# Kernel optimization log

Measured on AMD Instinct MI355X. Metric: run time of the kernel, lower is better.

Reference implementation:

```python
import jax, jax.numpy as jnp
import numpy as np

N, E, D, C, H1 = 50000, 800000, 128, 8, 2


def setup_inputs() -> dict:
    key = jax.random.key(0)
    ks = jax.random.split(key, 14)
    s = lambda k, sh: (jax.random.normal(k, sh, jnp.float32) * 0.05)
    return {
        "x": jax.random.normal(ks[0], (N, D), jnp.float32),
        "edge_index": jax.random.randint(ks[1], (2, E), 0, N, dtype=jnp.int32),
        # conv1: GATConv(D, D, heads=2, concat=True)
        "W1": s(ks[2], (D, H1 * D)),
        "att1_src": s(ks[3], (H1, D)),
        "att1_dst": s(ks[4], (H1, D)),
        "b1": s(ks[5], (H1 * D,)),
        # conv2: GATConv(2D, D, heads=1, concat=False)
        "W2": s(ks[6], (H1 * D, D)),
        "att2_src": s(ks[7], (1, D)),
        "att2_dst": s(ks[8], (1, D)),
        "b2": s(ks[9], (D,)),
        # MLP head
        "Wm1": s(ks[10], (D, D)),
        "bm1": s(ks[11], (D,)),
        "Wm2": s(ks[12], (D, C)),
        "bm2": s(ks[13], (C,)),
    }


def gat_conv(x, src, dst, W, a_src, a_dst, b, heads, out_ch, concat):
    """PyG GATConv (eval mode): self-loops added by caller, softmax over
    edges grouped by destination node, negative_slope=0.2."""
    n = x.shape[0]
    h = (x @ W).reshape(n, heads, out_ch)              # [N,H,F]
    alpha_src = jnp.einsum('nhf,hf->nh', h, a_src)     # [N,H]
    alpha_dst = jnp.einsum('nhf,hf->nh', h, a_dst)     # [N,H]
    e = jax.nn.leaky_relu(alpha_src[src] + alpha_dst[dst], 0.2)  # [E,H]
    e_max = jax.ops.segment_max(e, dst, num_segments=n)
    ex = jnp.exp(e - e_max[dst])
    denom = jax.ops.segment_sum(ex, dst, num_segments=n)
    alpha = ex / jnp.maximum(denom[dst], 1e-16)        # [E,H]
    out = jax.ops.segment_sum(h[src] * alpha[:, :, None], dst, num_segments=n)
    out = out.reshape(n, heads * out_ch) if concat else out.mean(axis=1)
    return out + b


def reference(x, edge_index, W1, att1_src, att1_dst, b1,
              W2, att2_src, att2_dst, b2, Wm1, bm1, Wm2, bm2):
    n = x.shape[0]
    loop = jnp.arange(n, dtype=edge_index.dtype)
    src = jnp.concatenate([edge_index[0], loop])  # add_self_loops=True
    dst = jnp.concatenate([edge_index[1], loop])
    h = jax.nn.elu(gat_conv(x, src, dst, W1, att1_src, att1_dst, b1, H1, D, True))
    h = jax.nn.elu(gat_conv(h, src, dst, W2, att2_src, att2_dst, b2, 1, D, False))
    h = jax.nn.relu(h @ Wm1 + bm1)
    return jax.nn.relu(h @ Wm2 + bm2)
```

## Files before the change

### kernel.cpp

```cpp
#include <hip/hip_runtime.h>
#include <hip/hip_bf16.h>


__device__ __forceinline__ float lrelu(float x){ return x > 0.f ? x : 0.2f*x; }
__device__ __forceinline__ float elu_f(float x){ return x > 0.f ? x : __expf(x) - 1.f; }
__device__ __forceinline__ unsigned short f2bf(float f){
  __hip_bfloat16 h = __float2bfloat16(f);
  return *reinterpret_cast<unsigned short*>(&h);
}
__device__ __forceinline__ float bflo(unsigned int u){ return __uint_as_float(u << 16); }
__device__ __forceinline__ float bfhi(unsigned int u){ return __uint_as_float(u & 0xffff0000u); }
__device__ __forceinline__ unsigned int packbf(float a, float b){
  return (unsigned int)f2bf(a) | ((unsigned int)f2bf(b) << 16);
}

typedef __attribute__((ext_vector_type(8))) short bf16x8;
typedef __attribute__((ext_vector_type(4))) float f32x4;

__global__ void prep_kernel(const float* __restrict__ W1, unsigned short* __restrict__ BT1a,
                            unsigned short* __restrict__ BT1b,
                            const float* __restrict__ W2, unsigned short* __restrict__ BT2,
                            const float* __restrict__ Wm1, unsigned short* __restrict__ BT3,
                            const float* __restrict__ a1s, const float* __restrict__ a1d,
                            float* __restrict__ va, int* __restrict__ bcount,
                            int* __restrict__ gcur, int NB){
  int idx = blockIdx.x*256 + threadIdx.x;
  const int S1 = 128*256, S2 = 128*256, S3 = 128*128;
  if (idx < S1){
    int k = idx >> 8, c = idx & 255;
    unsigned short v = f2bf(W1[idx]);
    if (c < 128) BT1a[c*128 + k] = v;
    else         BT1b[(c-128)*128 + k] = v;
  } else if (idx < S1 + S2){
    int j = idx - S1;
    int k = j >> 7, n = j & 127;
    BT2[n*256 + k] = f2bf(W2[j]);
  } else if (idx < S1 + S2 + S3){
    int j = idx - S1 - S2;
    int k = j >> 7, n = j & 127;
    BT3[n*128 + k] = f2bf(Wm1[j]);
  } else if (idx < S1 + S2 + S3 + 512){
    int j = idx - S1 - S2 - S3;
    int v = j >> 7, k = j & 127;
    const float* avec = (v < 2) ? a1s : a1d;
    int head = v & 1;
    const float4* wrow = (const float4*)(W1 + (size_t)k*256 + head*128);
    const float4* arow = (const float4*)(avec + head*128);
    float s = 0.f;
    #pragma unroll 8
    for (int f = 0; f < 32; ++f){
      float4 w = wrow[f], a = arow[f];
      s += w.x*a.x + w.y*a.y + w.z*a.z + w.w*a.w;
    }
    va[j] = s;
  } else if (idx < S1 + S2 + S3 + 512 + 2048){
    int z = idx - (S1 + S2 + S3 + 512);
    if (z < 1024){ if (z < NB) bcount[z] = 0; }
    else { z -= 1024; if (z < NB) gcur[z] = 0; }
  }
}

__global__ __launch_bounds__(256) void f2bf_hist_kernel(
    const float* __restrict__ x, unsigned short* __restrict__ xb, int N,
    const float* __restrict__ va, float* __restrict__ as1, float* __restrict__ ad1,
    const int* __restrict__ dst, int E, int* __restrict__ bcount, int NB, int nbConv)
{
  __shared__ int h[1024];
  if ((int)blockIdx.x < nbConv){
    int i = blockIdx.x*256 + threadIdx.x;
    int total = N*32;
    float4 v = make_float4(0.f,0.f,0.f,0.f);
    if (i < total){
      v = ((const float4*)x)[i];
      ushort4 u; u.x=f2bf(v.x); u.y=f2bf(v.y); u.z=f2bf(v.z); u.w=f2bf(v.w);
      ((ushort4*)xb)[i] = u;
    }
    int c = (i & 31) << 2;
    float4 vs0 = *(const float4*)(va + c);
    float4 vs1 = *(const float4*)(va + 128 + c);
    float4 vd0 = *(const float4*)(va + 256 + c);
    float4 vd1 = *(const float4*)(va + 384 + c);
    float s0 = v.x*vs0.x + v.y*vs0.y + v.z*vs0.z + v.w*vs0.w;
    float s1 = v.x*vs1.x + v.y*vs1.y + v.z*vs1.z + v.w*vs1.w;
    float d0 = v.x*vd0.x + v.y*vd0.y + v.z*vd0.z + v.w*vd0.w;
    float d1 = v.x*vd1.x + v.y*vd1.y + v.z*vd1.z + v.w*vd1.w;
    #pragma unroll
    for (int m = 1; m <= 16; m <<= 1){
      s0 += __shfl_xor(s0, m); s1 += __shfl_xor(s1, m);
      d0 += __shfl_xor(d0, m); d1 += __shfl_xor(d1, m);
    }
    if ((i & 31) == 0 && i < total){
      int n = i >> 5;
      *(float2*)(as1 + 2*n) = make_float2(s0, s1);
      *(float2*)(ad1 + 2*n) = make_float2(d0, d1);
    }
  } else {
    for (int i = threadIdx.x; i < NB; i += 256) h[i] = 0;
    __syncthreads();
    int b0 = blockIdx.x - nbConv;
    for (int e = b0*256 + threadIdx.x; e < E; e += 64*256)
      atomicAdd(&h[dst[e] >> 6], 1);
    __syncthreads();
    for (int i = threadIdx.x; i < NB; i += 256)
      if (h[i]) atomicAdd(&bcount[i], h[i]);
  }
}

__global__ __launch_bounds__(256) void bscatter_kernel(
    const int* __restrict__ src, const int* __restrict__ dst, int E,
    const int* __restrict__ bcount, int* __restrict__ boff,
    int* __restrict__ gcur, unsigned int* __restrict__ pairs, int NB)
{
  __shared__ int h[1024];
  __shared__ int runbase[1024];
  __shared__ int sc[1024];
  const int t = threadIdx.x;
  const int e0 = blockIdx.x * 4096;

  for (int i = t; i < 1024; i += 256) sc[i] = (i < NB) ? bcount[i] : 0;
  for (int i = t; i < NB; i += 256) h[i] = 0;
  __syncthreads();
  for (int d = 1; d < 1024; d <<= 1){
    int v0 = (t       >= d) ? sc[t       - d] : 0;
    int v1 = (t + 256 >= d) ? sc[t + 256 - d] : 0;
    int v2 = (t + 512 >= d) ? sc[t + 512 - d] : 0;
    int v3 = (t + 768 >= d) ? sc[t + 768 - d] : 0;
    __syncthreads();
    sc[t] += v0; sc[t+256] += v1; sc[t+512] += v2; sc[t+768] += v3;
    __syncthreads();
  }
  if (blockIdx.x == 0){
    for (int i = t; i <= NB; i += 256) boff[i] = i ? sc[i-1] : 0;
  }

  int myb[16]; unsigned int myw[16];
  #pragma unroll
  for (int q = 0; q < 16; ++q){
    int e = e0 + q*256 + t;
    int b = -1; unsigned int w = 0;
    if (e < E){
      int d = dst[e];
      b = d >> 6;
      w = ((unsigned int)(d & 63) << 26) | (unsigned int)src[e];
      atomicAdd(&h[b], 1);
    }
    myb[q] = b; myw[q] = w;
  }
  __syncthreads();
  for (int i = t; i < NB; i += 256)
    runbase[i] = h[i] ? atomicAdd(&gcur[i], h[i]) : 0;
  __syncthreads();
  for (int i = t; i < NB; i += 256) h[i] = 0;
  __syncthreads();
  #pragma unroll
  for (int q = 0; q < 16; ++q){
    if (myb[q] >= 0){
      int off = atomicAdd(&h[myb[q]], 1);
      int base = myb[q] ? sc[myb[q]-1] : 0;
      pairs[(size_t)base + runbase[myb[q]] + off] = myw[q];
    }
  }
}

__global__ __launch_bounds__(256) void bbuild_kernel(
    const unsigned int* __restrict__ pairs, const int* __restrict__ boff,
    int* __restrict__ rowptr, int* __restrict__ csr, int N)
{
  __shared__ int deg[64], offs[64], cur[64];
  const int b = blockIdx.x;
  const int t = threadIdx.x;
  const int n0 = b << 6;
  const int nNodes = min(64, N - n0);
  const int p0 = boff[b], p1 = boff[b+1];
  const int base = p0 + n0;
  if (t < 64) deg[t] = (t < nNodes) ? 1 : 0;
  __syncthreads();
  for (int i = p0 + t; i < p1; i += 256)
    atomicAdd(&deg[pairs[i] >> 26], 1);
  __syncthreads();
  if (t < 64){
    int x = deg[t];
    #pragma unroll
    for (int d = 1; d < 64; d <<= 1){
      int y = __shfl_up(x, d);
      if (t >= d) x += y;
    }
    offs[t] = x - deg[t];
    cur[t] = 1;
    if (t < nNodes){
      rowptr[n0 + t + 1] = base + x;
      csr[base + x - deg[t]] = n0 + t;
    }
    if (b == 0 && t == 0) rowptr[0] = 0;
  }
  __syncthreads();
  for (int i = p0 + t; i < p1; i += 256){
    unsigned int w = pairs[i];
    int dl = w >> 26;
    int s  = (int)(w & 0x03ffffffu);
    int off = atomicAdd(&cur[dl], 1);
    csr[base + offs[dl] + off] = s;
  }
}

__device__ __forceinline__ void gemm_core(
    const unsigned short* __restrict__ A, int lda,
    const unsigned short* __restrict__ BT, int M, int K, int r0,
    unsigned short* a_s, unsigned short* b_s, f32x4 (&acc)[4][4])
{
  const int tid  = threadIdx.x;
  const int lane = tid & 63, wv = tid >> 6;
  const int mh = (wv & 1)*64, nh = (wv >> 1)*64;
  const int l15 = lane & 15, quad = lane >> 4;
  const int srow = tid >> 3, skc = tid & 7;

  #pragma unroll
  for (int i = 0; i < 4; ++i)
    #pragma unroll
    for (int j = 0; j < 4; ++j)
      #pragma unroll
      for (int r = 0; r < 4; ++r) acc[i][j][r] = 0.f;

  for (int k0 = 0; k0 < K; k0 += 64){
    #pragma unroll
    for (int it = 0; it < 4; ++it){
      int row = it*32 + srow;
      int grow = r0 + row;
      uint4 v = make_uint4(0u,0u,0u,0u);
      if (grow < M) v = *(const uint4*)(A + (size_t)grow*lda + k0 + skc*8);
      *(uint4*)(&a_s[row*72 + skc*8]) = v;
    }
    #pragma unroll
    for (int it = 0; it < 4; ++it){
      int row = it*32 + srow;
      uint4 v = *(const uint4*)(BT + (size_t)row*K + k0 + skc*8);
      *(uint4*)(&b_s[row*72 + skc*8]) = v;
    }
    __syncthreads();
    #pragma unroll
    for (int ks = 0; ks < 64; ks += 32){
      bf16x8 af[4], bfr[4];
      #pragma unroll
      for (int i = 0; i < 4; ++i)
        af[i] = *(const bf16x8*)(&a_s[(mh + i*16 + l15)*72 + ks + quad*8]);
      #pragma unroll
      for (int j = 0; j < 4; ++j)
        bfr[j] = *(const bf16x8*)(&b_s[(nh + j*16 + l15)*72 + ks + quad*8]);
      #pragma unroll
      for (int i = 0; i < 4; ++i)
        #pragma unroll
        for (int j = 0; j < 4; ++j)
          acc[i][j] = __builtin_amdgcn_mfma_f32_16x16x32_bf16(bfr[j], af[i], acc[i][j], 0, 0, 0);
    }
    __syncthreads();
  }
}

__global__ __launch_bounds__(256) void gemm_conv1_kernel(
    const unsigned short* __restrict__ xa, const unsigned short* __restrict__ BT1a,
    const unsigned short* __restrict__ BT1b, unsigned short* __restrict__ out1b,
    int M, const float* __restrict__ b1)
{
  __shared__ unsigned short a_s[128*72];
  __shared__ unsigned short b_s[128*72];
  const int hx = blockIdx.x;
  const unsigned short* A  = xa + hx*128;
  const unsigned short* BT = hx ? BT1b : BT1a;
  unsigned short* C = out1b + hx*128;
  const float* bias = b1 + hx*128;
  const int r0 = blockIdx.y*128;
  f32x4 acc[4][4];
  gemm_core(A, 256, BT, M, 128, r0, a_s, b_s, acc);

  const int lane = threadIdx.x & 63, wv = threadIdx.x >> 6;
  const int mh = (wv & 1)*64, nh = (wv >> 1)*64;
  const int l15 = lane & 15, quad = lane >> 4;
  #pragma unroll
  for (int i = 0; i < 4; ++i){
    int m = r0 + mh + i*16 + l15;
    if (m < M){
      #pragma unroll
      for (int j = 0; j < 4; ++j){
        int n = nh + j*16 + quad*4;
        float4 bb = *(const float4*)(bias + n);
        ushort4 u;
        u.x = f2bf(elu_f(acc[i][j][0] + bb.x));
        u.y = f2bf(elu_f(acc[i][j][1] + bb.y));
        u.z = f2bf(elu_f(acc[i][j][2] + bb.z));
        u.w = f2bf(elu_f(acc[i][j][3] + bb.w));
        *(ushort4*)(C + (size_t)m*256 + n) = u;
      }
    }
  }
}

__global__ __launch_bounds__(256) void gemm_conv2_kernel(
    const unsigned short* __restrict__ out1b, const unsigned short* __restrict__ BT2,
    unsigned short* __restrict__ h2b, int M,
    const float* __restrict__ a2s, const float* __restrict__ a2d,
    float* __restrict__ as2, float* __restrict__ ad2)
{
  __shared__ unsigned short a_s[128*72];
  __shared__ unsigned short b_s[128*72];
  __shared__ float part_s[128][2];
  __shared__ float part_d[128][2];
  const int r0 = blockIdx.y*128;
  f32x4 acc[4][4];
  gemm_core(out1b, 256, BT2, M, 256, r0, a_s, b_s, acc);

  const int tid = threadIdx.x;
  const int lane = tid & 63, wv = tid >> 6;
  const int mh = (wv & 1)*64, nh = (wv >> 1)*64;
  const int l15 = lane & 15, quad = lane >> 4;
  #pragma unroll
  for (int i = 0; i < 4; ++i){
    int m = r0 + mh + i*16 + l15;
    float ps = 0.f, pd = 0.f;
    #pragma unroll
    for (int j = 0; j < 4; ++j){
      int n = nh + j*16 + quad*4;
      float4 wsv = *(const float4*)(a2s + n);
      float4 wdv = *(const float4*)(a2d + n);
      float v0 = acc[i][j][0], v1 = acc[i][j][1], v2 = acc[i][j][2], v3 = acc[i][j][3];
      ps += v0*wsv.x + v1*wsv.y + v2*wsv.z + v3*wsv.w;
      pd += v0*wdv.x + v1*wdv.y + v2*wdv.z + v3*wdv.w;
      if (m < M){
        ushort4 u;
        u.x = f2bf(v0); u.y = f2bf(v1); u.z = f2bf(v2); u.w = f2bf(v3);
        *(ushort4*)(h2b + (size_t)m*128 + n) = u;
      }
    }
    ps += __shfl_xor(ps, 16); ps += __shfl_xor(ps, 32);
    pd += __shfl_xor(pd, 16); pd += __shfl_xor(pd, 32);
    if (quad == 0){
      part_s[mh + i*16 + l15][wv >> 1] = ps;
      part_d[mh + i*16 + l15][wv >> 1] = pd;
    }
  }
  __syncthreads();
  if (tid < 128){
    int gm = r0 + tid;
    if (gm < M){
      as2[gm] = part_s[tid][0] + part_s[tid][1];
      ad2[gm] = part_d[tid][0] + part_d[tid][1];
    }
  }
}

__global__ __launch_bounds__(256) void gemm_mlp_kernel(
    const unsigned short* __restrict__ gb, const unsigned short* __restrict__ BT3,
    int M, const float* __restrict__ bm1, const float* __restrict__ Wm2,
    const float* __restrict__ bm2, float* __restrict__ out)
{
  __shared__ unsigned short a_s[128*72];
  __shared__ unsigned short b_s[128*72];
  __shared__ float wm2_s[128*8];
  __shared__ float part[128][2][8];
  const int tid = threadIdx.x;
  {
    int i4 = tid*4;
    *(float4*)(&wm2_s[i4]) = *(const float4*)(Wm2 + i4);
  }
  const int r0 = blockIdx.y*128;
  f32x4 acc[4][4];
  gemm_core(gb, 128, BT3, M, 128, r0, a_s, b_s, acc);

  const int lane = tid & 63, wv = tid >> 6;
  const int mh = (wv & 1)*64, nh = (wv >> 1)*64;
  const int l15 = lane & 15, quad = lane >> 4;
  #pragma unroll
  for (int i = 0; i < 4; ++i){
    float po[8];
    #pragma unroll
    for (int o = 0; o < 8; ++o) po[o] = 0.f;
    #pragma unroll
    for (int j = 0; j < 4; ++j){
      int n = nh + j*16 + quad*4;
      float4 bb = *(const float4*)(bm1 + n);
      #pragma unroll
      for (int r = 0; r < 4; ++r){
        float hcol = fmaxf(acc[i][j][r] + ((const float*)&bb)[r], 0.f);
        const float* wr = &wm2_s[(n + r)*8];
        #pragma unroll
        for (int o = 0; o < 8; ++o) po[o] += hcol*wr[o];
      }
    }
    #pragma unroll
    for (int o = 0; o < 8; ++o){
      po[o] += __shfl_xor(po[o], 16);
      po[o] += __shfl_xor(po[o], 32);
    }
    if (quad == 0){
      #pragma unroll
      for (int o = 0; o < 8; ++o) part[mh + i*16 + l15][wv >> 1][o] = po[o];
    }
  }
  __syncthreads();
  if (tid < 128){
    int gm = r0 + tid;
    if (gm < M){
      float4 o0, o1;
      o0.x = fmaxf(part[tid][0][0] + part[tid][1][0] + bm2[0], 0.f);
      o0.y = fmaxf(part[tid][0][1] + part[tid][1][1] + bm2[1], 0.f);
      o0.z = fmaxf(part[tid][0][2] + part[tid][1][2] + bm2[2], 0.f);
      o0.w = fmaxf(part[tid][0][3] + part[tid][1][3] + bm2[3], 0.f);
      o1.x = fmaxf(part[tid][0][4] + part[tid][1][4] + bm2[4], 0.f);
      o1.y = fmaxf(part[tid][0][5] + part[tid][1][5] + bm2[5], 0.f);
      o1.z = fmaxf(part[tid][0][6] + part[tid][1][6] + bm2[6], 0.f);
      o1.w = fmaxf(part[tid][0][7] + part[tid][1][7] + bm2[7], 0.f);
      *(float4*)(out + (size_t)gm*8)     = o0;
      *(float4*)(out + (size_t)gm*8 + 4) = o1;
    }
  }
}

#define AGG1_FMA(u, a0v, a1v) do{ \
    float f0 = bflo(u.x), f1 = bfhi(u.x), f2v = bflo(u.y), f3 = bfhi(u.y); \
    float f4 = bflo(u.z), f5 = bfhi(u.z), f6 = bflo(u.w), f7 = bfhi(u.w); \
    acc0[0] += a0v*f0; acc0[1] += a0v*f1; acc0[2] += a0v*f2v; acc0[3] += a0v*f3; \
    acc0[4] += a0v*f4; acc0[5] += a0v*f5; acc0[6] += a0v*f6;  acc0[7] += a0v*f7; \
    acc1[0] += a1v*f0; acc1[1] += a1v*f1; acc1[2] += a1v*f2v; acc1[3] += a1v*f3; \
    acc1[4] += a1v*f4; acc1[5] += a1v*f5; acc1[6] += a1v*f6;  acc1[7] += a1v*f7; \
  }while(0)

#define AGG2_FMA(u, av) do{ \
    acc[0] += av*bflo(u.x); acc[1] += av*bfhi(u.x); \
    acc[2] += av*bflo(u.y); acc[3] += av*bfhi(u.y); \
    acc[4] += av*bflo(u.z); acc[5] += av*bfhi(u.z); \
    acc[6] += av*bflo(u.w); acc[7] += av*bfhi(u.w); \
  }while(0)

__global__ __launch_bounds__(256) void agg1x_kernel(
    const unsigned short* __restrict__ xb, const float* __restrict__ as_,
    const float* __restrict__ ad_, const int* __restrict__ rowptr, const int* __restrict__ csr,
    unsigned short* __restrict__ xa, int N)
{
  const int wv = threadIdx.x >> 6, lane = threadIdx.x & 63;
  const int ql = lane & 15;
  const int n = blockIdx.x*16 + wv*4 + (lane >> 4);
  const bool valid = n < N;
  int start = 0, end = 0;
  float2 adv = make_float2(0.f, 0.f);
  if (valid){ start = rowptr[n]; end = rowptr[n+1]; adv = *(const float2*)(ad_ + 2*n); }

  int jl = start + ql;
  bool have = valid && (jl < end);
  int s_l = 0;
  float p0 = 0.f, p1 = 0.f;
  if (have){
    s_l = csr[jl];
    float2 av = *(const float2*)(as_ + 2*s_l);
    p0 = __expf(lrelu(av.x + adv.x));
    p1 = __expf(lrelu(av.y + adv.y));
  }
  float l0 = p0, l1 = p1;
  for (int j = jl + 16; j < end; j += 16){
    int s = csr[j];
    float2 av = *(const float2*)(as_ + 2*s);
    l0 += __expf(lrelu(av.x + adv.x));
    l1 += __expf(lrelu(av.y + adv.y));
  }
  #pragma unroll
  for (int msk = 1; msk <= 8; msk <<= 1){
    l0 += __shfl_xor(l0, msk);
    l1 += __shfl_xor(l1, msk);
  }
  float inv0 = 1.f / fmaxf(l0, 1e-16f);
  float inv1 = 1.f / fmaxf(l1, 1e-16f);
  float a0_l = p0 * inv0;
  float a1_l = p1 * inv1;

  float acc0[8], acc1[8];
  #pragma unroll
  for (int i = 0; i < 8; ++i){ acc0[i] = 0.f; acc1[i] = 0.f; }
  const int c = ql << 3;
  const unsigned short* hp = xb + c;

  #pragma unroll
  for (int t = 0; t < 16; t += 2){
    int   sA  = __shfl(s_l, t, 16),   sB  = __shfl(s_l, t+1, 16);
    float a0A = __shfl(a0_l, t, 16),  a0B = __shfl(a0_l, t+1, 16);
    float a1A = __shfl(a1_l, t, 16),  a1B = __shfl(a1_l, t+1, 16);
    uint4 uA = *(const uint4*)(hp + (sA << 7));
    uint4 uB = *(const uint4*)(hp + (sB << 7));
    AGG1_FMA(uA, a0A, a1A);
    AGG1_FMA(uB, a0B, a1B);
  }
  for (int jb = start + 16; jb < end; jb += 16){
    int jl2 = jb + ql;
    int s2 = 0; float a0_2 = 0.f, a1_2 = 0.f;
    if (jl2 < end){
      s2 = csr[jl2];
      float2 av = *(const float2*)(as_ + 2*s2);
      a0_2 = __expf(lrelu(av.x + adv.x)) * inv0;
      a1_2 = __expf(lrelu(av.y + adv.y)) * inv1;
    }
    int cnt2 = min(16, end - jb);
    for (int t2 = 0; t2 < cnt2; t2 += 2){
      int   sA  = __shfl(s2, t2, 16),   sB  = __shfl(s2, t2+1, 16);
      float a0A = __shfl(a0_2, t2, 16), a0B = __shfl(a0_2, t2+1, 16);
      float a1A = __shfl(a1_2, t2, 16), a1B = __shfl(a1_2, t2+1, 16);
      uint4 uA = *(const uint4*)(hp + (sA << 7));
      uint4 uB = *(const uint4*)(hp + (sB << 7));
      AGG1_FMA(uA, a0A, a1A);
      AGG1_FMA(uB, a0B, a1B);
    }
  }

  if (valid){
    uint4 u0, u1;
    u0.x = packbf(acc0[0], acc0[1]); u0.y = packbf(acc0[2], acc0[3]);
    u0.z = packbf(acc0[4], acc0[5]); u0.w = packbf(acc0[6], acc0[7]);
    u1.x = packbf(acc1[0], acc1[1]); u1.y = packbf(acc1[2], acc1[3]);
    u1.z = packbf(acc1[4], acc1[5]); u1.w = packbf(acc1[6], acc1[7]);
    *(uint4*)(xa + (size_t)n*256 + c)       = u0;
    *(uint4*)(xa + (size_t)n*256 + 128 + c) = u1;
  }
}

__global__ __launch_bounds__(256) void agg2_kernel(
    const unsigned short* __restrict__ h2b, const float* __restrict__ as_,
    const float* __restrict__ ad_, const int* __restrict__ rowptr, const int* __restrict__ csr,
    const float* __restrict__ b2, unsigned short* __restrict__ outb, int N)
{
  const int wv = threadIdx.x >> 6, lane = threadIdx.x & 63;
  const int ql = lane & 15;
  const int n = blockIdx.x*16 + wv*4 + (lane >> 4);
  const bool valid = n < N;
  int start = 0, end = 0;
  float adn = 0.f;
  if (valid){ start = rowptr[n]; end = rowptr[n+1]; adn = ad_[n]; }

  int jl = start + ql;
  bool have = valid && (jl < end);
  int s_l = 0;
  float p_l = 0.f;
  if (have){
    s_l = csr[jl];
    p_l = __expf(lrelu(as_[s_l] + adn));
  }
  float l = p_l;
  for (int j = jl + 16; j < end; j += 16)
    l += __expf(lrelu(as_[csr[j]] + adn));
  #pragma unroll
  for (int msk = 1; msk <= 8; msk <<= 1) l += __shfl_xor(l, msk);
  float inv = 1.f / fmaxf(l, 1e-16f);
  float a_l = p_l * inv;

  float acc[8];
  #pragma unroll
  for (int i = 0; i < 8; ++i) acc[i] = 0.f;
  const int c = ql << 3;
  const unsigned short* hp = h2b + c;

  #pragma unroll
  for (int t = 0; t < 16; t += 2){
    int   sA = __shfl(s_l, t, 16),  sB = __shfl(s_l, t+1, 16);
    float aA = __shfl(a_l, t, 16),  aB = __shfl(a_l, t+1, 16);
    uint4 uA = *(const uint4*)(hp + (sA << 7));
    uint4 uB = *(const uint4*)(hp + (sB << 7));
    AGG2_FMA(uA, aA);
    AGG2_FMA(uB, aB);
  }
  for (int jb = start + 16; jb < end; jb += 16){
    int jl2 = jb + ql;
    int s2 = 0; float a2 = 0.f;
    if (jl2 < end){
      s2 = csr[jl2];
      a2 = __expf(lrelu(as_[s2] + adn)) * inv;
    }
    int cnt2 = min(16, end - jb);
    for (int t2 = 0; t2 < cnt2; t2 += 2){
      int   sA = __shfl(s2, t2, 16),  sB = __shfl(s2, t2+1, 16);
      float aA = __shfl(a2, t2, 16),  aB = __shfl(a2, t2+1, 16);
      uint4 uA = *(const uint4*)(hp + (sA << 7));
      uint4 uB = *(const uint4*)(hp + (sB << 7));
      AGG2_FMA(uA, aA);
      AGG2_FMA(uB, aB);
    }
  }

  if (valid){
    float4 bb0 = *(const float4*)(b2 + c);
    float4 bb1 = *(const float4*)(b2 + c + 4);
    float o[8];
    o[0]=elu_f(acc[0]+bb0.x); o[1]=elu_f(acc[1]+bb0.y);
    o[2]=elu_f(acc[2]+bb0.z); o[3]=elu_f(acc[3]+bb0.w);
    o[4]=elu_f(acc[4]+bb1.x); o[5]=elu_f(acc[5]+bb1.y);
    o[6]=elu_f(acc[6]+bb1.z); o[7]=elu_f(acc[7]+bb1.w);
    uint4 up;
    up.x = packbf(o[0], o[1]); up.y = packbf(o[2], o[3]);
    up.z = packbf(o[4], o[5]); up.w = packbf(o[6], o[7]);
    *(uint4*)(outb + (size_t)n*128 + c) = up;
  }
}

extern "C" void kernel_launch(void* const* d_in, const int* in_sizes, int n_in,
                              void* d_out, int out_size, void* d_ws, size_t ws_size,
                              hipStream_t stream)
{
  (void)n_in; (void)out_size; (void)ws_size;
  const float* x   = (const float*)d_in[0];
  const int*   ei  = (const int*)d_in[1];
  const float* W1  = (const float*)d_in[2];
  const float* a1s = (const float*)d_in[3];
  const float* a1d = (const float*)d_in[4];
  const float* b1  = (const float*)d_in[5];
  const float* W2  = (const float*)d_in[6];
  const float* a2s = (const float*)d_in[7];
  const float* a2d = (const float*)d_in[8];
  const float* b2  = (const float*)d_in[9];
  const float* Wm1 = (const float*)d_in[10];
  const float* bm1 = (const float*)d_in[11];
  const float* Wm2 = (const float*)d_in[12];
  const float* bm2 = (const float*)d_in[13];
  float* out = (float*)d_out;

  const int N = in_sizes[0] / 128;
  const int E = in_sizes[1] / 2;
  const int NB = (N + 63) >> 6;
  const int* srcp = ei;
  const int* dstp = ei + E;

  char* ws = (char*)d_ws;
  unsigned short* xb    = (unsigned short*)ws;
  unsigned short* xa    = (unsigned short*)(ws + (size_t)N*256);
  unsigned short* out1b = (unsigned short*)(ws + (size_t)N*768);
  unsigned short* h2b   = (unsigned short*)(ws + (size_t)N*1280);
  char* tail = ws + (size_t)N*1536;
  unsigned short* BT1a = (unsigned short*)tail;
  unsigned short* BT1b = BT1a + 128*128;
  unsigned short* BT2  = BT1b + 128*128;
  unsigned short* BT3  = BT2 + 128*256;
  float* va   = (float*)(BT3 + 128*128);
  float* as1  = va + 512;
  float* ad1  = as1 + (size_t)2*N;
  float* as2  = ad1 + (size_t)2*N;
  float* ad2  = as2 + N;
  int* bcount = (int*)(ad2 + N);
  int* boff   = bcount + 1024;
  int* gcur   = boff + 1032;
  int* rowptr = gcur + 1024;
  int* csr    = rowptr + N + 1;
  unsigned int* pairs = (unsigned int*)(csr + E + N);

  unsigned short* gb = xb;

  const int nbConv = (N*32 + 255)/256;
  const int prepTotal = 128*256 + 128*256 + 128*128 + 512 + 2048;

  prep_kernel<<<(prepTotal + 255)/256, 256, 0, stream>>>(
      W1, BT1a, BT1b, W2, BT2, Wm1, BT3, a1s, a1d, va, bcount, gcur, NB);
  f2bf_hist_kernel<<<nbConv + 64, 256, 0, stream>>>(x, xb, N, va, as1, ad1,
                                                    dstp, E, bcount, NB, nbConv);
  bscatter_kernel<<<(E + 4095)/4096, 256, 0, stream>>>(srcp, dstp, E, bcount, boff, gcur, pairs, NB);
  bbuild_kernel<<<NB, 256, 0, stream>>>(pairs, boff, rowptr, csr, N);

  const int gy   = (N + 127) / 128;
  const int nb16 = (N + 15) / 16;

  agg1x_kernel<<<nb16, 256, 0, stream>>>(xb, as1, ad1, rowptr, csr, xa, N);
  gemm_conv1_kernel<<<dim3(2, gy), 256, 0, stream>>>(xa, BT1a, BT1b, out1b, N, b1);
  gemm_conv2_kernel<<<dim3(1, gy), 256, 0, stream>>>(out1b, BT2, h2b, N, a2s, a2d, as2, ad2);
  agg2_kernel<<<nb16, 256, 0, stream>>>(h2b, as2, ad2, rowptr, csr, b2, gb, N);
  gemm_mlp_kernel<<<dim3(1, gy), 256, 0, stream>>>(gb, BT3, N, bm1, Wm2, bm2, out);
}
```

Baseline: 264.5 us.

## Fuse edge aggregation with following GEMMs via shared-memory tiles

Merges the conv1 aggregation kernel with the conv1 GEMM and the conv2 aggregation kernel with the MLP GEMM. Each 64-row block aggregates neighbour features into LDS, then runs MFMA against weight fragments read directly from global memory. This removes the global round trips of the aggregated xa and gb intermediates and two launches. In exchange, the smaller 64-row tiles re-read the weight matrices from global or L2 per block, and the gather phase may suffer lower occupancy because of the larger LDS footprint.

Result: slower. 319.7 us (+20.9%).

```diff
diff --git a/kernel.cpp b/kernel.cpp
--- a/kernel.cpp
+++ b/kernel.cpp
@@ -256,44 +256,6 @@
   }
 }
 
-__global__ __launch_bounds__(256) void gemm_conv1_kernel(
-    const unsigned short* __restrict__ xa, const unsigned short* __restrict__ BT1a,
-    const unsigned short* __restrict__ BT1b, unsigned short* __restrict__ out1b,
-    int M, const float* __restrict__ b1)
-{
-  __shared__ unsigned short a_s[128*72];
-  __shared__ unsigned short b_s[128*72];
-  const int hx = blockIdx.x;
-  const unsigned short* A  = xa + hx*128;
-  const unsigned short* BT = hx ? BT1b : BT1a;
-  unsigned short* C = out1b + hx*128;
-  const float* bias = b1 + hx*128;
-  const int r0 = blockIdx.y*128;
-  f32x4 acc[4][4];
-  gemm_core(A, 256, BT, M, 128, r0, a_s, b_s, acc);
-
-  const int lane = threadIdx.x & 63, wv = threadIdx.x >> 6;
-  const int mh = (wv & 1)*64, nh = (wv >> 1)*64;
-  const int l15 = lane & 15, quad = lane >> 4;
-  #pragma unroll
-  for (int i = 0; i < 4; ++i){
-    int m = r0 + mh + i*16 + l15;
-    if (m < M){
-      #pragma unroll
-      for (int j = 0; j < 4; ++j){
-        int n = nh + j*16 + quad*4;
-        float4 bb = *(const float4*)(bias + n);
-        ushort4 u;
-        u.x = f2bf(elu_f(acc[i][j][0] + bb.x));
-        u.y = f2bf(elu_f(acc[i][j][1] + bb.y));
-        u.z = f2bf(elu_f(acc[i][j][2] + bb.z));
-        u.w = f2bf(elu_f(acc[i][j][3] + bb.w));
-        *(ushort4*)(C + (size_t)m*256 + n) = u;
-      }
-    }
-  }
-}
-
 __global__ __launch_bounds__(256) void gemm_conv2_kernel(
     const unsigned short* __restrict__ out1b, const unsigned short* __restrict__ BT2,
     unsigned short* __restrict__ h2b, int M,
@@ -347,40 +309,295 @@
   }
 }
 
-__global__ __launch_bounds__(256) void gemm_mlp_kernel(
-    const unsigned short* __restrict__ gb, const unsigned short* __restrict__ BT3,
-    int M, const float* __restrict__ bm1, const float* __restrict__ Wm2,
-    const float* __restrict__ bm2, float* __restrict__ out)
+#define AGG1_FMA(u, a0v, a1v) do{ \
+    float f0 = bflo(u.x), f1 = bfhi(u.x), f2v = bflo(u.y), f3 = bfhi(u.y); \
+    float f4 = bflo(u.z), f5 = bfhi(u.z), f6 = bflo(u.w), f7 = bfhi(u.w); \
+    acc0[0] += a0v*f0; acc0[1] += a0v*f1; acc0[2] += a0v*f2v; acc0[3] += a0v*f3; \
+    acc0[4] += a0v*f4; acc0[5] += a0v*f5; acc0[6] += a0v*f6;  acc0[7] += a0v*f7; \
+    acc1[0] += a1v*f0; acc1[1] += a1v*f1; acc1[2] += a1v*f2v; acc1[3] += a1v*f3; \
+    acc1[4] += a1v*f4; acc1[5] += a1v*f5; acc1[6] += a1v*f6;  acc1[7] += a1v*f7; \
+  }while(0)
+
+#define AGG2_FMA(u, av) do{ \
+    acc[0] += av*bflo(u.x); acc[1] += av*bfhi(u.x); \
+    acc[2] += av*bflo(u.y); acc[3] += av*bfhi(u.y); \
+    acc[4] += av*bflo(u.z); acc[5] += av*bfhi(u.z); \
+    acc[6] += av*bflo(u.w); acc[7] += av*bfhi(u.w); \
+  }while(0)
+
+__global__ __launch_bounds__(256) void agg1gemm_kernel(
+    const unsigned short* __restrict__ xb, const float* __restrict__ as_,
+    const float* __restrict__ ad_, const int* __restrict__ rowptr, const int* __restrict__ csr,
+    const unsigned short* __restrict__ BT1a, const unsigned short* __restrict__ BT1b,
+    const float* __restrict__ b1, unsigned short* __restrict__ out1b, int N)
 {
-  __shared__ unsigned short a_s[128*72];
-  __shared__ unsigned short b_s[128*72];
+  __shared__ unsigned short xa_s[64*264];
+  const int tid = threadIdx.x;
+  const int g = tid >> 4;
+  const int ql = tid & 15;
+  const int r0 = blockIdx.x*64;
+  const int c = ql << 3;
+  const unsigned short* hp = xb + c;
+
+  for (int rr = 0; rr < 4; ++rr){
+    const int row = g*4 + rr;
+    const int n = r0 + row;
+    const bool valid = n < N;
+    int start = 0, end = 0;
+    float2 adv = make_float2(0.f, 0.f);
+    if (valid){ start = rowptr[n]; end = rowptr[n+1]; adv = *(const float2*)(ad_ + 2*n); }
+
+    int jl = start + ql;
+    bool have = valid && (jl < end);
+    int s_l = 0;
+    float p0 = 0.f, p1 = 0.f;
+    if (have){
+      s_l = csr[jl];
+      float2 av = *(const float2*)(as_ + 2*s_l);
+      p0 = __expf(lrelu(av.x + adv.x));
+      p1 = __expf(lrelu(av.y + adv.y));
+    }
+    float l0 = p0, l1 = p1;
+    for (int j = jl + 16; j < end; j += 16){
+      int s = csr[j];
+      float2 av = *(const float2*)(as_ + 2*s);
+      l0 += __expf(lrelu(av.x + adv.x));
+      l1 += __expf(lrelu(av.y + adv.y));
+    }
+    #pragma unroll
+    for (int msk = 1; msk <= 8; msk <<= 1){
+      l0 += __shfl_xor(l0, msk);
+      l1 += __shfl_xor(l1, msk);
+    }
+    float inv0 = 1.f / fmaxf(l0, 1e-16f);
+    float inv1 = 1.f / fmaxf(l1, 1e-16f);
+    float a0_l = p0 * inv0;
+    float a1_l = p1 * inv1;
+
+    float acc0[8], acc1[8];
+    #pragma unroll
+    for (int i = 0; i < 8; ++i){ acc0[i] = 0.f; acc1[i] = 0.f; }
+
+    #pragma unroll
+    for (int t = 0; t < 16; t += 2){
+      int   sA  = __shfl(s_l, t, 16),   sB  = __shfl(s_l, t+1, 16);
+      float a0A = __shfl(a0_l, t, 16),  a0B = __shfl(a0_l, t+1, 16);
+      float a1A = __shfl(a1_l, t, 16),  a1B = __shfl(a1_l, t+1, 16);
+      uint4 uA = *(const uint4*)(hp + (sA << 7));
+      uint4 uB = *(const uint4*)(hp + (sB << 7));
+      AGG1_FMA(uA, a0A, a1A);
+      AGG1_FMA(uB, a0B, a1B);
+    }
+    for (int jb = start + 16; jb < end; jb += 16){
+      int jl2 = jb + ql;
+      int s2 = 0; float a0_2 = 0.f, a1_2 = 0.f;
+      if (jl2 < end){
+        s2 = csr[jl2];
+        float2 av = *(const float2*)(as_ + 2*s2);
+        a0_2 = __expf(lrelu(av.x + adv.x)) * inv0;
+        a1_2 = __expf(lrelu(av.y + adv.y)) * inv1;
+      }
+      int cnt2 = min(16, end - jb);
+      for (int t2 = 0; t2 < cnt2; t2 += 2){
+        int   sA  = __shfl(s2, t2, 16),   sB  = __shfl(s2, t2+1, 16);
+        float a0A = __shfl(a0_2, t2, 16), a0B = __shfl(a0_2, t2+1, 16);
+        float a1A = __shfl(a1_2, t2, 16), a1B = __shfl(a1_2, t2+1, 16);
+        uint4 uA = *(const uint4*)(hp + (sA << 7));
+        uint4 uB = *(const uint4*)(hp + (sB << 7));
+        AGG1_FMA(uA, a0A, a1A);
+        AGG1_FMA(uB, a0B, a1B);
+      }
+    }
+
+    uint4 u0, u1;
+    u0.x = packbf(acc0[0], acc0[1]); u0.y = packbf(acc0[2], acc0[3]);
+    u0.z = packbf(acc0[4], acc0[5]); u0.w = packbf(acc0[6], acc0[7]);
+    u1.x = packbf(acc1[0], acc1[1]); u1.y = packbf(acc1[2], acc1[3]);
+    u1.z = packbf(acc1[4], acc1[5]); u1.w = packbf(acc1[6], acc1[7]);
+    *(uint4*)(&xa_s[row*264 + c])       = u0;
+    *(uint4*)(&xa_s[row*264 + 128 + c]) = u1;
+  }
+  __syncthreads();
+
+  const int lane = tid & 63, wv = tid >> 6;
+  const int rh = (wv & 1)*32;
+  const int h  = wv >> 1;
+  const unsigned short* BT = h ? BT1b : BT1a;
+  const int l15 = lane & 15, quad = lane >> 4;
+  f32x4 acc[2][8];
+  #pragma unroll
+  for (int i = 0; i < 2; ++i)
+    #pragma unroll
+    for (int j = 0; j < 8; ++j)
+      #pragma unroll
+      for (int r = 0; r < 4; ++r) acc[i][j][r] = 0.f;
+
+  #pragma unroll
+  for (int ks = 0; ks < 128; ks += 32){
+    bf16x8 af[2], bfr[8];
+    #pragma unroll
+    for (int i = 0; i < 2; ++i)
+      af[i] = *(const bf16x8*)(&xa_s[(rh + i*16 + l15)*264 + h*128 + ks + quad*8]);
+    #pragma unroll
+    for (int j = 0; j < 8; ++j)
+      bfr[j] = *(const bf16x8*)(BT + (size_t)(j*16 + l15)*128 + ks + quad*8);
+    #pragma unroll
+    for (int i = 0; i < 2; ++i)
+      #pragma unroll
+      for (int j = 0; j < 8; ++j)
+        acc[i][j] = __builtin_amdgcn_mfma_f32_16x16x32_bf16(bfr[j], af[i], acc[i][j], 0, 0, 0);
+  }
+
+  const float* bias = b1 + h*128;
+  #pragma unroll
+  for (int i = 0; i < 2; ++i){
+    int m = r0 + rh + i*16 + l15;
+    if (m < N){
+      #pragma unroll
+      for (int j = 0; j < 8; ++j){
+        int nn = j*16 + quad*4;
+        float4 bb = *(const float4*)(bias + nn);
+        ushort4 u;
+        u.x = f2bf(elu_f(acc[i][j][0] + bb.x));
+        u.y = f2bf(elu_f(acc[i][j][1] + bb.y));
+        u.z = f2bf(elu_f(acc[i][j][2] + bb.z));
+        u.w = f2bf(elu_f(acc[i][j][3] + bb.w));
+        *(ushort4*)(out1b + (size_t)m*256 + h*128 + nn) = u;
+      }
+    }
+  }
+}
+
+__global__ __launch_bounds__(256) void agg2mlp_kernel(
+    const unsigned short* __restrict__ h2b, const float* __restrict__ as_,
+    const float* __restrict__ ad_, const int* __restrict__ rowptr, const int* __restrict__ csr,
+    const float* __restrict__ b2, const unsigned short* __restrict__ BT3,
+    const float* __restrict__ bm1, const float* __restrict__ Wm2,
+    const float* __restrict__ bm2, float* __restrict__ out, int N)
+{
+  __shared__ unsigned short gb_s[64*136];
   __shared__ float wm2_s[128*8];
-  __shared__ float part[128][2][8];
+  __shared__ float part[64][2][8];
   const int tid = threadIdx.x;
   {
     int i4 = tid*4;
     *(float4*)(&wm2_s[i4]) = *(const float4*)(Wm2 + i4);
   }
-  const int r0 = blockIdx.y*128;
-  f32x4 acc[4][4];
-  gemm_core(gb, 128, BT3, M, 128, r0, a_s, b_s, acc);
+  const int g = tid >> 4;
+  const int ql = tid & 15;
+  const int r0 = blockIdx.x*64;
+  const int c = ql << 3;
+  const unsigned short* hp = h2b + c;
+
+  for (int rr = 0; rr < 4; ++rr){
+    const int row = g*4 + rr;
+    const int n = r0 + row;
+    const bool valid = n < N;
+    int start = 0, end = 0;
+    float adn = 0.f;
+    if (valid){ start = rowptr[n]; end = rowptr[n+1]; adn = ad_[n]; }
+
+    int jl = start + ql;
+    bool have = valid && (jl < end);
+    int s_l = 0;
+    float p_l = 0.f;
+    if (have){
+      s_l = csr[jl];
+      p_l = __expf(lrelu(as_[s_l] + adn));
+    }
+    float l = p_l;
+    for (int j = jl + 16; j < end; j += 16)
+      l += __expf(lrelu(as_[csr[j]] + adn));
+    #pragma unroll
+    for (int msk = 1; msk <= 8; msk <<= 1) l += __shfl_xor(l, msk);
+    float inv = 1.f / fmaxf(l, 1e-16f);
+    float a_l = p_l * inv;
+
+    float acc[8];
+    #pragma unroll
+    for (int i = 0; i < 8; ++i) acc[i] = 0.f;
+
+    #pragma unroll
+    for (int t = 0; t < 16; t += 2){
+      int   sA = __shfl(s_l, t, 16),  sB = __shfl(s_l, t+1, 16);
+      float aA = __shfl(a_l, t, 16),  aB = __shfl(a_l, t+1, 16);
+      uint4 uA = *(const uint4*)(hp + (sA << 7));
+      uint4 uB = *(const uint4*)(hp + (sB << 7));
+      AGG2_FMA(uA, aA);
+      AGG2_FMA(uB, aB);
+    }
+    for (int jb = start + 16; jb < end; jb += 16){
+      int jl2 = jb + ql;
+      int s2 = 0; float a2 = 0.f;
+      if (jl2 < end){
+        s2 = csr[jl2];
+        a2 = __expf(lrelu(as_[s2] + adn)) * inv;
+      }
+      int cnt2 = min(16, end - jb);
+      for (int t2 = 0; t2 < cnt2; t2 += 2){
+        int   sA = __shfl(s2, t2, 16),  sB = __shfl(s2, t2+1, 16);
+        float aA = __shfl(a2, t2, 16),  aB = __shfl(a2, t2+1, 16);
+        uint4 uA = *(const uint4*)(hp + (sA << 7));
+        uint4 uB = *(const uint4*)(hp + (sB << 7));
+        AGG2_FMA(uA, aA);
+        AGG2_FMA(uB, aB);
+      }
+    }
+
+    float4 bb0 = *(const float4*)(b2 + c);
+    float4 bb1 = *(const float4*)(b2 + c + 4);
+    float o[8];
+    o[0]=elu_f(acc[0]+bb0.x); o[1]=elu_f(acc[1]+bb0.y);
+    o[2]=elu_f(acc[2]+bb0.z); o[3]=elu_f(acc[3]+bb0.w);
+    o[4]=elu_f(acc[4]+bb1.x); o[5]=elu_f(acc[5]+bb1.y);
+    o[6]=elu_f(acc[6]+bb1.z); o[7]=elu_f(acc[7]+bb1.w);
+    uint4 up;
+    up.x = packbf(o[0], o[1]); up.y = packbf(o[2], o[3]);
+    up.z = packbf(o[4], o[5]); up.w = packbf(o[6], o[7]);
+    *(uint4*)(&gb_s[row*136 + c]) = up;
+  }
+  __syncthreads();
 
   const int lane = tid & 63, wv = tid >> 6;
-  const int mh = (wv & 1)*64, nh = (wv >> 1)*64;
+  const int rh = (wv & 1)*32, nh = (wv >> 1)*64;
   const int l15 = lane & 15, quad = lane >> 4;
-  #pragma unroll
-  for (int i = 0; i < 4; ++i){
+  f32x4 acc[2][4];
+  #pragma unroll
+  for (int i = 0; i < 2; ++i)
+    #pragma unroll
+    for (int j = 0; j < 4; ++j)
+      #pragma unroll
+      for (int r = 0; r < 4; ++r) acc[i][j][r] = 0.f;
+
+  #pragma unroll
+  for (int ks = 0; ks < 128; ks += 32){
+    bf16x8 af[2], bfr[4];
+    #pragma unroll
+    for (int i = 0; i < 2; ++i)
+      af[i] = *(const bf16x8*)(&gb_s[(rh + i*16 + l15)*136 + ks + quad*8]);
+    #pragma unroll
+    for (int j = 0; j < 4; ++j)
+      bfr[j] = *(const bf16x8*)(BT3 + (size_t)(nh + j*16 + l15)*128 + ks + quad*8);
+    #pragma unroll
+    for (int i = 0; i < 2; ++i)
+      #pragma unroll
+      for (int j = 0; j < 4; ++j)
+        acc[i][j] = __builtin_amdgcn_mfma_f32_16x16x32_bf16(bfr[j], af[i], acc[i][j], 0, 0, 0);
+  }
+
+  #pragma unroll
+  for (int i = 0; i < 2; ++i){
     float po[8];
     #pragma unroll
     for (int o = 0; o < 8; ++o) po[o] = 0.f;
     #pragma unroll
     for (int j = 0; j < 4; ++j){
-      int n = nh + j*16 + quad*4;
-      float4 bb = *(const float4*)(bm1 + n);
+      int nn = nh + j*16 + quad*4;
+      float4 bb = *(const float4*)(bm1 + nn);
       #pragma unroll
       for (int r = 0; r < 4; ++r){
         float hcol = fmaxf(acc[i][j][r] + ((const float*)&bb)[r], 0.f);
-        const float* wr = &wm2_s[(n + r)*8];
+        const float* wr = &wm2_s[(nn + r)*8];
         #pragma unroll
         for (int o = 0; o < 8; ++o) po[o] += hcol*wr[o];
       }
@@ -392,13 +609,13 @@
     }
     if (quad == 0){
       #pragma unroll
-      for (int o = 0; o < 8; ++o) part[mh + i*16 + l15][wv >> 1][o] = po[o];
-    }
-  }
-  __syncthreads();
-  if (tid < 128){
+      for (int o = 0; o < 8; ++o) part[rh + i*16 + l15][wv >> 1][o] = po[o];
+    }
+  }
+  __syncthreads();
+  if (tid < 64){
     int gm = r0 + tid;
-    if (gm < M){
+    if (gm < N){
       float4 o0, o1;
       o0.x = fmaxf(part[tid][0][0] + part[tid][1][0] + bm2[0], 0.f);
       o0.y = fmaxf(part[tid][0][1] + part[tid][1][1] + bm2[1], 0.f);
@@ -411,187 +628,6 @@
       *(float4*)(out + (size_t)gm*8)     = o0;
       *(float4*)(out + (size_t)gm*8 + 4) = o1;
     }
-  }
-}
-
-#define AGG1_FMA(u, a0v, a1v) do{ \
-    float f0 = bflo(u.x), f1 = bfhi(u.x), f2v = bflo(u.y), f3 = bfhi(u.y); \
-    float f4 = bflo(u.z), f5 = bfhi(u.z), f6 = bflo(u.w), f7 = bfhi(u.w); \
-    acc0[0] += a0v*f0; acc0[1] += a0v*f1; acc0[2] += a0v*f2v; acc0[3] += a0v*f3; \
-    acc0[4] += a0v*f4; acc0[5] += a0v*f5; acc0[6] += a0v*f6;  acc0[7] += a0v*f7; \
-    acc1[0] += a1v*f0; acc1[1] += a1v*f1; acc1[2] += a1v*f2v; acc1[3] += a1v*f3; \
-    acc1[4] += a1v*f4; acc1[5] += a1v*f5; acc1[6] += a1v*f6;  acc1[7] += a1v*f7; \
-  }while(0)
-
-#define AGG2_FMA(u, av) do{ \
-    acc[0] += av*bflo(u.x); acc[1] += av*bfhi(u.x); \
-    acc[2] += av*bflo(u.y); acc[3] += av*bfhi(u.y); \
-    acc[4] += av*bflo(u.z); acc[5] += av*bfhi(u.z); \
-    acc[6] += av*bflo(u.w); acc[7] += av*bfhi(u.w); \
-  }while(0)
-
-__global__ __launch_bounds__(256) void agg1x_kernel(
-    const unsigned short* __restrict__ xb, const float* __restrict__ as_,
-    const float* __restrict__ ad_, const int* __restrict__ rowptr, const int* __restrict__ csr,
-    unsigned short* __restrict__ xa, int N)
-{
-  const int wv = threadIdx.x >> 6, lane = threadIdx.x & 63;
-  const int ql = lane & 15;
-  const int n = blockIdx.x*16 + wv*4 + (lane >> 4);
-  const bool valid = n < N;
-  int start = 0, end = 0;
-  float2 adv = make_float2(0.f, 0.f);
-  if (valid){ start = rowptr[n]; end = rowptr[n+1]; adv = *(const float2*)(ad_ + 2*n); }
-
-  int jl = start + ql;
-  bool have = valid && (jl < end);
-  int s_l = 0;
-  float p0 = 0.f, p1 = 0.f;
-  if (have){
-    s_l = csr[jl];
-    float2 av = *(const float2*)(as_ + 2*s_l);
-    p0 = __expf(lrelu(av.x + adv.x));
-    p1 = __expf(lrelu(av.y + adv.y));
-  }
-  float l0 = p0, l1 = p1;
-  for (int j = jl + 16; j < end; j += 16){
-    int s = csr[j];
-    float2 av = *(const float2*)(as_ + 2*s);
-    l0 += __expf(lrelu(av.x + adv.x));
-    l1 += __expf(lrelu(av.y + adv.y));
-  }
-  #pragma unroll
-  for (int msk = 1; msk <= 8; msk <<= 1){
-    l0 += __shfl_xor(l0, msk);
-    l1 += __shfl_xor(l1, msk);
-  }
-  float inv0 = 1.f / fmaxf(l0, 1e-16f);
-  float inv1 = 1.f / fmaxf(l1, 1e-16f);
-  float a0_l = p0 * inv0;
-  float a1_l = p1 * inv1;
-
-  float acc0[8], acc1[8];
-  #pragma unroll
-  for (int i = 0; i < 8; ++i){ acc0[i] = 0.f; acc1[i] = 0.f; }
-  const int c = ql << 3;
-  const unsigned short* hp = xb + c;
-
-  #pragma unroll
-  for (int t = 0; t < 16; t += 2){
-    int   sA  = __shfl(s_l, t, 16),   sB  = __shfl(s_l, t+1, 16);
-    float a0A = __shfl(a0_l, t, 16),  a0B = __shfl(a0_l, t+1, 16);
-    float a1A = __shfl(a1_l, t, 16),  a1B = __shfl(a1_l, t+1, 16);
-    uint4 uA = *(const uint4*)(hp + (sA << 7));
-    uint4 uB = *(const uint4*)(hp + (sB << 7));
-    AGG1_FMA(uA, a0A, a1A);
-    AGG1_FMA(uB, a0B, a1B);
-  }
-  for (int jb = start + 16; jb < end; jb += 16){
-    int jl2 = jb + ql;
-    int s2 = 0; float a0_2 = 0.f, a1_2 = 0.f;
-    if (jl2 < end){
-      s2 = csr[jl2];
-      float2 av = *(const float2*)(as_ + 2*s2);
-      a0_2 = __expf(lrelu(av.x + adv.x)) * inv0;
-      a1_2 = __expf(lrelu(av.y + adv.y)) * inv1;
-    }
-    int cnt2 = min(16, end - jb);
-    for (int t2 = 0; t2 < cnt2; t2 += 2){
-      int   sA  = __shfl(s2, t2, 16),   sB  = __shfl(s2, t2+1, 16);
-      float a0A = __shfl(a0_2, t2, 16), a0B = __shfl(a0_2, t2+1, 16);
-      float a1A = __shfl(a1_2, t2, 16), a1B = __shfl(a1_2, t2+1, 16);
-      uint4 uA = *(const uint4*)(hp + (sA << 7));
-      uint4 uB = *(const uint4*)(hp + (sB << 7));
-      AGG1_FMA(uA, a0A, a1A);
-      AGG1_FMA(uB, a0B, a1B);
-    }
-  }
-
-  if (valid){
-    uint4 u0, u1;
-    u0.x = packbf(acc0[0], acc0[1]); u0.y = packbf(acc0[2], acc0[3]);
-    u0.z = packbf(acc0[4], acc0[5]); u0.w = packbf(acc0[6], acc0[7]);
-    u1.x = packbf(acc1[0], acc1[1]); u1.y = packbf(acc1[2], acc1[3]);
-    u1.z = packbf(acc1[4], acc1[5]); u1.w = packbf(acc1[6], acc1[7]);
-    *(uint4*)(xa + (size_t)n*256 + c)       = u0;
-    *(uint4*)(xa + (size_t)n*256 + 128 + c) = u1;
-  }
-}
-
-__global__ __launch_bounds__(256) void agg2_kernel(
-    const unsigned short* __restrict__ h2b, const float* __restrict__ as_,
-    const float* __restrict__ ad_, const int* __restrict__ rowptr, const int* __restrict__ csr,
-    const float* __restrict__ b2, unsigned short* __restrict__ outb, int N)
-{
-  const int wv = threadIdx.x >> 6, lane = threadIdx.x & 63;
-  const int ql = lane & 15;
-  const int n = blockIdx.x*16 + wv*4 + (lane >> 4);
-  const bool valid = n < N;
-  int start = 0, end = 0;
-  float adn = 0.f;
-  if (valid){ start = rowptr[n]; end = rowptr[n+1]; adn = ad_[n]; }
-
-  int jl = start + ql;
-  bool have = valid && (jl < end);
-  int s_l = 0;
-  float p_l = 0.f;
-  if (have){
-    s_l = csr[jl];
-    p_l = __expf(lrelu(as_[s_l] + adn));
-  }
-  float l = p_l;
-  for (int j = jl + 16; j < end; j += 16)
-    l += __expf(lrelu(as_[csr[j]] + adn));
-  #pragma unroll
-  for (int msk = 1; msk <= 8; msk <<= 1) l += __shfl_xor(l, msk);
-  float inv = 1.f / fmaxf(l, 1e-16f);
-  float a_l = p_l * inv;
-
-  float acc[8];
-  #pragma unroll
-  for (int i = 0; i < 8; ++i) acc[i] = 0.f;
-  const int c = ql << 3;
-  const unsigned short* hp = h2b + c;
-
-  #pragma unroll
-  for (int t = 0; t < 16; t += 2){
-    int   sA = __shfl(s_l, t, 16),  sB = __shfl(s_l, t+1, 16);
-    float aA = __shfl(a_l, t, 16),  aB = __shfl(a_l, t+1, 16);
-    uint4 uA = *(const uint4*)(hp + (sA << 7));
-    uint4 uB = *(const uint4*)(hp + (sB << 7));
-    AGG2_FMA(uA, aA);
-    AGG2_FMA(uB, aB);
-  }
-  for (int jb = start + 16; jb < end; jb += 16){
-    int jl2 = jb + ql;
-    int s2 = 0; float a2 = 0.f;
-    if (jl2 < end){
-      s2 = csr[jl2];
-      a2 = __expf(lrelu(as_[s2] + adn)) * inv;
-    }
-    int cnt2 = min(16, end - jb);
-    for (int t2 = 0; t2 < cnt2; t2 += 2){
-      int   sA = __shfl(s2, t2, 16),  sB = __shfl(s2, t2+1, 16);
-      float aA = __shfl(a2, t2, 16),  aB = __shfl(a2, t2+1, 16);
-      uint4 uA = *(const uint4*)(hp + (sA << 7));
-      uint4 uB = *(const uint4*)(hp + (sB << 7));
-      AGG2_FMA(uA, aA);
-      AGG2_FMA(uB, aB);
-    }
-  }
-
-  if (valid){
-    float4 bb0 = *(const float4*)(b2 + c);
-    float4 bb1 = *(const float4*)(b2 + c + 4);
-    float o[8];
-    o[0]=elu_f(acc[0]+bb0.x); o[1]=elu_f(acc[1]+bb0.y);
-    o[2]=elu_f(acc[2]+bb0.z); o[3]=elu_f(acc[3]+bb0.w);
-    o[4]=elu_f(acc[4]+bb1.x); o[5]=elu_f(acc[5]+bb1.y);
-    o[6]=elu_f(acc[6]+bb1.z); o[7]=elu_f(acc[7]+bb1.w);
-    uint4 up;
-    up.x = packbf(o[0], o[1]); up.y = packbf(o[2], o[3]);
-    up.z = packbf(o[4], o[5]); up.w = packbf(o[6], o[7]);
-    *(uint4*)(outb + (size_t)n*128 + c) = up;
   }
 }
 
@@ -624,10 +660,9 @@
 
   char* ws = (char*)d_ws;
   unsigned short* xb    = (unsigned short*)ws;
-  unsigned short* xa    = (unsigned short*)(ws + (size_t)N*256);
-  unsigned short* out1b = (unsigned short*)(ws + (size_t)N*768);
-  unsigned short* h2b   = (unsigned short*)(ws + (size_t)N*1280);
-  char* tail = ws + (size_t)N*1536;
+  unsigned short* out1b = (unsigned short*)(ws + (size_t)N*256);
+  unsigned short* h2b   = (unsigned short*)(ws + (size_t)N*768);
+  char* tail = ws + (size_t)N*1024;
   unsigned short* BT1a = (unsigned short*)tail;
   unsigned short* BT1b = BT1a + 128*128;
   unsigned short* BT2  = BT1b + 128*128;
@@ -644,8 +679,6 @@
   int* csr    = rowptr + N + 1;
   unsigned int* pairs = (unsigned int*)(csr + E + N);
 
-  unsigned short* gb = xb;
-
   const int nbConv = (N*32 + 255)/256;
   const int prepTotal = 128*256 + 128*256 + 128*128 + 512 + 2048;
 
@@ -656,12 +689,12 @@
   bscatter_kernel<<<(E + 4095)/4096, 256, 0, stream>>>(srcp, dstp, E, bcount, boff, gcur, pairs, NB);
   bbuild_kernel<<<NB, 256, 0, stream>>>(pairs, boff, rowptr, csr, N);
 
-  const int gy   = (N + 127) / 128;
-  const int nb16 = (N + 15) / 16;
-
-  agg1x_kernel<<<nb16, 256, 0, stream>>>(xb, as1, ad1, rowptr, csr, xa, N);
-  gemm_conv1_kernel<<<dim3(2, gy), 256, 0, stream>>>(xa, BT1a, BT1b, out1b, N, b1);
+  const int g64 = (N + 63) / 64;
+  const int gy  = (N + 127) / 128;
+
+  agg1gemm_kernel<<<g64, 256, 0, stream>>>(xb, as1, ad1, rowptr, csr,
+                                           BT1a, BT1b, b1, out1b, N);
   gemm_conv2_kernel<<<dim3(1, gy), 256, 0, stream>>>(out1b, BT2, h2b, N, a2s, a2d, as2, ad2);
-  agg2_kernel<<<nb16, 256, 0, stream>>>(h2b, as2, ad2, rowptr, csr, b2, gb, N);
-  gemm_mlp_kernel<<<dim3(1, gy), 256, 0, stream>>>(gb, BT3, N, bm1, Wm2, bm2, out);
-}
+  agg2mlp_kernel<<<g64, 256, 0, stream>>>(h2b, as2, ad2, rowptr, csr,
+                                          b2, BT3, bm1, Wm2, bm2, out, N);
+}
```
